# Performance work log

Measured on AMD Instinct MI355X. Metric: run time of the kernel, lower is better.

Reference implementation:

```python
import jax, jax.numpy as jnp
import numpy as np

L, P, DV, DP = 16, 1024, 64, 16   # latent caps, prim caps (neighbors), latent vec, prim vec
N_SRC, N_TGT = 64, 64
NUM_ITER = 3


def setup_inputs() -> dict:
    key = jax.random.key(0)
    k1, k2, k3 = jax.random.split(key, 3)
    feature = jax.random.normal(k1, (N_SRC + N_TGT, DP), dtype=jnp.float32)
    # neighbor indices: each half indexes into its own 64-row feature block
    select_cap = jax.random.randint(k2, (N_SRC + N_TGT, P), 0, N_SRC).astype(jnp.int64)
    W = 0.01 * jax.random.normal(k3, (L, P, DV, DP), dtype=jnp.float32)
    return {"feature": feature, "select_cap": select_cap, "W": W, "n_src": N_SRC}


def squash(s):
    # s: [..., DV]
    sn = jnp.sum(s * s, axis=-1, keepdims=True)
    return sn * s / ((1.0 + sn) * jnp.sqrt(sn))


def routing(x, W):
    # x: [B, P, DP], W: [L, P, DV, DP]
    u_hat = jnp.einsum('lpvq,bpq->blpv', W, x)          # [B, L, P, DV]
    u_det = jax.lax.stop_gradient(u_hat)                 # matches torch .detach()
    b = jnp.zeros(x.shape[:1] + (L, P), dtype=x.dtype)   # routing logits [B, L, P]
    for _ in range(NUM_ITER - 1):
        c = jax.nn.softmax(b, axis=1)                    # softmax over latent caps dim
        v = squash(jnp.einsum('blp,blpv->blv', c, u_det))
        b = b + jnp.einsum('blv,blpv->blp', v, u_det)
    c = jax.nn.softmax(b, axis=1)
    return squash(jnp.einsum('blp,blpv->blv', c, u_hat))  # [B, L, DV]


def reference(feature, select_cap, W, n_src):
    # per-point neighbor gather, honoring src/tgt split at n_src
    feat_src = feature[:n_src]
    feat_tgt = feature[n_src:]
    batch_src = feat_src[select_cap[:n_src]]             # [n_src, P, DP]
    batch_tgt = feat_tgt[select_cap[n_src:]]             # [n_tgt, P, DP]
    batch_feat = jnp.concatenate([batch_src, batch_tgt], axis=0)  # [N, P, DP]
    caps = routing(batch_feat, W)                        # [N, L, DV]
    norms = jnp.linalg.norm(caps, axis=-1).T             # [L, N]
    return caps, norms
```

## Files before the change

### kernel.cpp

```cpp
#include <hip/hip_runtime.h>
#include <hip/hip_fp16.h>

namespace {

constexpr int L_  = 16;
constexpr int P_  = 1024;
constexpr int DV_ = 64;
constexpr int DP_ = 16;
constexpr int B_  = 128;

constexpr size_t PB   = (size_t)P_ * B_;
constexpr size_t SLV  = (size_t)B_ * L_ * DV_;
constexpr size_t LPBT = (size_t)L_ * PB;

constexpr int KCH = 64;
constexpr int PPC = P_ / KCH;

typedef _Float16 f16;
typedef __attribute__((ext_vector_type(4)))  _Float16 f16x4;
typedef __attribute__((ext_vector_type(8)))  _Float16 f16x8;
typedef __attribute__((ext_vector_type(16))) float    f32x16;

constexpr size_t WF_UNITS = (size_t)L_ * P_ * 2 * 64;

__device__ __forceinline__ f16x8 mul_pk(const __half2 cwh, const f16x8 f) {
  union { f16x8 v; __half2 h2[4]; } fu, bu;
  fu.v = f;
#pragma unroll
  for (int i = 0; i < 4; ++i) bu.h2[i] = __hmul2(cwh, fu.h2[i]);
  return bu.v;
}

__global__ __launch_bounds__(256) void k_prepcvt(
    const float* __restrict__ W, const float* __restrict__ feat,
    const int* __restrict__ sel, const int* __restrict__ nsrc_p,
    f16* __restrict__ wf, f16* __restrict__ xq, f16* __restrict__ xqs)
{
  const int bid = blockIdx.x, tid = threadIdx.x;
  if (bid < 8192) {
    const int l   = bid & 15;
    const int rem = (bid >> 4) * 256 + tid;
    const int lane = rem & 63;
    const int mt   = (rem >> 6) & 1;
    const int p    = rem >> 7;
    const int v  = mt * 32 + (lane & 31);
    const int q8 = (lane >> 5) * 8;
    const float* src = W + (((size_t)l * P_ + p) * 64 + v) * 16 + q8;
    const float4 a = *(const float4*)src;
    const float4 b = *(const float4*)(src + 4);
    union { f16x8 v8; __half2 h2[4]; } o;
    o.h2[0] = __float22half2_rn(float2{a.x, a.y});
    o.h2[1] = __float22half2_rn(float2{a.z, a.w});
    o.h2[2] = __float22half2_rn(float2{b.x, b.y});
    o.h2[3] = __float22half2_rn(float2{b.z, b.w});
    reinterpret_cast<f16x8*>(wf)[(size_t)l * 131072 + rem] = o.v8;
  } else {
    const int id2 = (bid - 8192) * 256 + tid;
    const int p = id2 >> 7, b = id2 & 127;
    const int ns = *nsrc_p;
    const int j = sel[b * P_ + p] + (b >= ns ? ns : 0);
    const float4 f0 = *(const float4*)(feat + j * DP_);
    const float4 f1 = *(const float4*)(feat + j * DP_ + 4);
    const float4 f2 = *(const float4*)(feat + j * DP_ + 8);
    const float4 f3 = *(const float4*)(feat + j * DP_ + 12);
    union { f16x8 v8; __half2 h2[4]; } u0, u1, s0, s1;
    u0.h2[0] = __float22half2_rn(float2{f0.x, f0.y});
    u0.h2[1] = __float22half2_rn(float2{f0.z, f0.w});
    u0.h2[2] = __float22half2_rn(float2{f1.x, f1.y});
    u0.h2[3] = __float22half2_rn(float2{f1.z, f1.w});
    u1.h2[0] = __float22half2_rn(float2{f2.x, f2.y});
    u1.h2[1] = __float22half2_rn(float2{f2.z, f2.w});
    u1.h2[2] = __float22half2_rn(float2{f3.x, f3.y});
    u1.h2[3] = __float22half2_rn(float2{f3.z, f3.w});
    const __half2 sc = __float2half2_rn(0.0625f);
#pragma unroll
    for (int i = 0; i < 4; ++i) {
      s0.h2[i] = __hmul2(sc, u0.h2[i]);
      s1.h2[i] = __hmul2(sc, u1.h2[i]);
    }
    f16x8* xqu  = reinterpret_cast<f16x8*>(xq);
    f16x8* xqsu = reinterpret_cast<f16x8*>(xqs);
    xqu[(size_t)id2 * 2]      = u0.v8;
    xqu[(size_t)id2 * 2 + 1]  = u1.v8;
    xqsu[(size_t)id2 * 2]     = s0.v8;
    xqsu[(size_t)id2 * 2 + 1] = s1.v8;
  }
}

template<bool UNIFORM>
__global__ __launch_bounds__(256, 4) void k_wsum(
    const f16* __restrict__ wf, const f16* __restrict__ xq,
    const f16* __restrict__ xqs, const f16* __restrict__ cbuf,
    f16* __restrict__ spart)
{
  const int bid  = blockIdx.x;
  const int l    = bid & 15;
  const int kc   = bid >> 4;
  const int wave = threadIdx.x >> 6;
  const int lane = threadIdx.x & 63;
  const int col  = lane & 31;
  const int h    = lane >> 5;
  const int bcol = wave * 32 + col;

  f32x16 accA0, accA1, accB0, accB1;
#pragma unroll
  for (int r = 0; r < 16; ++r) {
    accA0[r] = 0.f; accA1[r] = 0.f; accB0[r] = 0.f; accB1[r] = 0.f;
  }

  const int p0 = kc * PPC;
  const f16x8* wfu = reinterpret_cast<const f16x8*>(wf);
  const f16x8* xqu = reinterpret_cast<const f16x8*>(UNIFORM ? xqs : xq);
#pragma unroll 4
  for (int ps = 0; ps < PPC; ++ps) {
    const int p = p0 + ps;
    const size_t lp = (size_t)l * P_ + p;

    f16x8 bfrag = xqu[(size_t)(p * B_ + bcol) * 2 + h];
    if (!UNIFORM) {
      const f16 cw = cbuf[(size_t)l * PB + (size_t)p * B_ + bcol];
      const __half hc = *reinterpret_cast<const __half*>(&cw);
      bfrag = mul_pk(__half2half2(hc), bfrag);
    }

    const f16x8 a0 = wfu[(lp * 2 + 0) * 64 + lane];
    const f16x8 a1 = wfu[(lp * 2 + 1) * 64 + lane];
    if (ps & 1) {
      accB0 = __builtin_amdgcn_mfma_f32_32x32x16_f16(a0, bfrag, accB0, 0, 0, 0);
      accB1 = __builtin_amdgcn_mfma_f32_32x32x16_f16(a1, bfrag, accB1, 0, 0, 0);
    } else {
      accA0 = __builtin_amdgcn_mfma_f32_32x32x16_f16(a0, bfrag, accA0, 0, 0, 0);
      accA1 = __builtin_amdgcn_mfma_f32_32x32x16_f16(a1, bfrag, accA1, 0, 0, 0);
    }
  }

  f16* op = spart + ((size_t)l * KCH + kc) * 8192 + (size_t)bcol * 64;
#pragma unroll
  for (int g = 0; g < 4; ++g) {
    f16x4 lo, hi;
#pragma unroll
    for (int j = 0; j < 4; ++j) {
      lo[j] = (f16)(accA0[g * 4 + j] + accB0[g * 4 + j]);
      hi[j] = (f16)(accA1[g * 4 + j] + accB1[g * 4 + j]);
    }
    *reinterpret_cast<f16x4*>(op + 8 * g + 4 * h)      = lo;
    *reinterpret_cast<f16x4*>(op + 32 + 8 * g + 4 * h) = hi;
  }
}

__global__ __launch_bounds__(256) void k_rsum(
    const f16* __restrict__ spart, float* __restrict__ sres)
{
  const int bid = blockIdx.x;
  const int l = bid & 15;
  const int r = bid >> 4;
  const int e = r * 1024 + threadIdx.x * 4;
  const f16* sp = spart + (size_t)l * KCH * 8192 + e;
  float a0 = 0.f, a1 = 0.f, a2 = 0.f, a3 = 0.f;
#pragma unroll
  for (int c = 0; c < KCH; ++c) {
    const f16x4 t = *reinterpret_cast<const f16x4*>(sp + (size_t)c * 8192);
    a0 += (float)t[0]; a1 += (float)t[1]; a2 += (float)t[2]; a3 += (float)t[3];
  }
  *reinterpret_cast<float4*>(sres + (size_t)l * 8192 + e) = float4{a0, a1, a2, a3};
}

template<bool ADDB>
__global__ __launch_bounds__(256, 4) void k_dotv(
    const f16* __restrict__ wf, const f16* __restrict__ xq,
    const float* __restrict__ sres, float* __restrict__ bb)
{
  const int bid  = blockIdx.x;
  const int l    = bid & 15;
  const int kc   = bid >> 4;
  const int wave = threadIdx.x >> 6;
  const int lane = threadIdx.x & 63;
  const int col  = lane & 31;
  const int h    = lane >> 5;
  const int bcol = wave * 32 + col;

  float vr0[16], vr1[16];
  float sn = 0.f;
  const float* vp = sres + (size_t)l * 8192 + (size_t)bcol * 64;
#pragma unroll
  for (int g = 0; g < 4; ++g) {
    const float4 lo = *reinterpret_cast<const float4*>(vp + 8 * g + 4 * h);
    const float4 hi = *reinterpret_cast<const float4*>(vp + 32 + 8 * g + 4 * h);
    vr0[g * 4 + 0] = lo.x; vr0[g * 4 + 1] = lo.y;
    vr0[g * 4 + 2] = lo.z; vr0[g * 4 + 3] = lo.w;
    vr1[g * 4 + 0] = hi.x; vr1[g * 4 + 1] = hi.y;
    vr1[g * 4 + 2] = hi.z; vr1[g * 4 + 3] = hi.w;
    sn += lo.x * lo.x + lo.y * lo.y + lo.z * lo.z + lo.w * lo.w;
    sn += hi.x * hi.x + hi.y * hi.y + hi.z * hi.z + hi.w * hi.w;
  }
  sn += __shfl_xor(sn, 32);
  const float scale = sqrtf(sn) / (1.f + sn);
#pragma unroll
  for (int r = 0; r < 16; ++r) { vr0[r] *= scale; vr1[r] *= scale; }

  f32x16 zz;
#pragma unroll
  for (int r = 0; r < 16; ++r) zz[r] = 0.f;

  const int p0 = kc * PPC;
  const f16x8* wfu = reinterpret_cast<const f16x8*>(wf);
  const f16x8* xqu = reinterpret_cast<const f16x8*>(xq);

#pragma unroll 2
  for (int ps = 0; ps < PPC; ++ps) {
    const int p = p0 + ps;
    const size_t lp = (size_t)l * P_ + p;

    const f16x8 bfrag = xqu[(size_t)(p * B_ + bcol) * 2 + h];
    const f16x8 a0 = wfu[(lp * 2 + 0) * 64 + lane];
    const f16x8 a1 = wfu[(lp * 2 + 1) * 64 + lane];
    const f32x16 u0 = __builtin_amdgcn_mfma_f32_32x32x16_f16(a0, bfrag, zz, 0, 0, 0);
    const f32x16 u1 = __builtin_amdgcn_mfma_f32_32x32x16_f16(a1, bfrag, zz, 0, 0, 0);

    float d = 0.f;
#pragma unroll
    for (int r = 0; r < 16; ++r) {
      d = fmaf(u0[r], vr0[r], d);
      d = fmaf(u1[r], vr1[r], d);
    }
    d += __shfl_xor(d, 32);
    if (h == 0) {
      const size_t o = (size_t)l * PB + (size_t)p * B_ + bcol;
      bb[o] = ADDB ? d + bb[o] : d;
    }
  }
}

__global__ __launch_bounds__(256) void k_softmax(
    const float* __restrict__ lin, f16* __restrict__ cout)
{
  const int idx = blockIdx.x * 256 + threadIdx.x;
  const float* ip = lin + idx;
  float x[L_];
  float m = -1e30f;
#pragma unroll
  for (int l = 0; l < L_; ++l) { x[l] = ip[(size_t)l * PB]; m = fmaxf(m, x[l]); }
  float den = 0.f;
#pragma unroll
  for (int l = 0; l < L_; ++l) { x[l] = __expf(x[l] - m); den += x[l]; }
  const float r = 1.f / den;
  f16* op = cout + idx;
#pragma unroll
  for (int l = 0; l < L_; ++l) op[(size_t)l * PB] = (f16)(x[l] * r);
}

__global__ __launch_bounds__(256) void k_squashF(
    const float* __restrict__ sres, float* __restrict__ caps,
    float* __restrict__ norms)
{
  const int bid = blockIdx.x;
  const int l = bid & 15;
  const int b = (bid >> 4) * 4 + (threadIdx.x >> 6);
  const int v = threadIdx.x & 63;

  const float x = sres[(size_t)l * 8192 + (size_t)b * 64 + v];
  float t2 = x * x;
#pragma unroll
  for (int m = 32; m >= 1; m >>= 1) t2 += __shfl_xor(t2, m, 64);
  const float scale = sqrtf(t2) / (1.f + t2);

  caps[((size_t)b * L_ + l) * DV_ + v] = x * scale;
  if (v == 0) norms[(size_t)l * B_ + b] = t2 / (1.f + t2);
}

}

extern "C" void kernel_launch(void* const* d_in, const int* in_sizes, int n_in,
                              void* d_out, int out_size, void* d_ws, size_t ws_size,
                              hipStream_t stream)
{
  (void)in_sizes; (void)n_in; (void)out_size; (void)ws_size;
  const float* feat   = (const float*)d_in[0];
  const int*   sel    = (const int*)d_in[1];
  const float* W      = (const float*)d_in[2];
  const int*   nsrc_p = (const int*)d_in[3];

  float* caps  = (float*)d_out;
  float* norms = caps + SLV;

  char* base = (char*)d_ws;
  f16*   wf     = (f16*)base;                         base += WF_UNITS * 8 * 2;
  f16*   spart  = (f16*)base;                         base += (size_t)L_ * KCH * 8192 * 2;
  float* sres   = (float*)base;                       base += (size_t)L_ * 8192 * 4;
  float* bb1    = (float*)base;                       base += LPBT * 4;
  f16*   cbuf16 = (f16*)base;                         base += LPBT * 2;
  f16*   xq     = (f16*)base;                         base += PB * DP_ * 2;
  f16*   xqs    = (f16*)base;

  const dim3 blk(256);
  const dim3 gP(8704);
  const dim3 gH(KCH * L_);
  const dim3 gRS(128);
  const dim3 gS(512);
  const dim3 gQ(512);

  k_prepcvt<<<gP, blk, 0, stream>>>(W, feat, sel, nsrc_p, wf, xq, xqs);

  k_wsum<true ><<<gH, blk, 0, stream>>>(wf, xq, xqs, nullptr, spart);
  k_rsum       <<<gRS, blk, 0, stream>>>(spart, sres);
  k_dotv<false><<<gH, blk, 0, stream>>>(wf, xq, sres, bb1);

  k_softmax    <<<gS, blk, 0, stream>>>(bb1, cbuf16);
  k_wsum<false><<<gH, blk, 0, stream>>>(wf, xq, xqs, cbuf16, spart);
  k_rsum       <<<gRS, blk, 0, stream>>>(spart, sres);
  k_dotv<true ><<<gH, blk, 0, stream>>>(wf, xq, sres, bb1);

  k_softmax    <<<gS, blk, 0, stream>>>(bb1, cbuf16);
  k_wsum<false><<<gH, blk, 0, stream>>>(wf, xq, xqs, cbuf16, spart);
  k_rsum       <<<gRS, blk, 0, stream>>>(spart, sres);
  k_squashF    <<<gQ, blk, 0, stream>>>(sres, caps, norms);
}
```

Measured before the change: 225.1 us.

## Drop pre-scaled feature copy, store routing logits in fp16, fuse final reduce with squash

The separate 1/16-scaled feature buffer is removed. The uniform first iteration now uses the unscaled features, and the 1/16 factor is applied to the summed vector when the first dot product runs. Routing logits are stored in fp16 rather than fp32, which halves the logit traffic in the dot and softmax kernels. The final partial-sum reduction is fused with the squash and norm output, removing one launch and the round trip through sres. It also reorders the prep kernel so the gather blocks come first. The risks are precision loss in the fp16 logits and possible overflow in the unscaled fp16 partial sums.

Result: faster. 220.4 us (-2.1%).

```diff
diff --git a/kernel.cpp b/kernel.cpp
--- a/kernel.cpp
+++ b/kernel.cpp
@@ -34,12 +34,34 @@
 __global__ __launch_bounds__(256) void k_prepcvt(
     const float* __restrict__ W, const float* __restrict__ feat,
     const int* __restrict__ sel, const int* __restrict__ nsrc_p,
-    f16* __restrict__ wf, f16* __restrict__ xq, f16* __restrict__ xqs)
+    f16* __restrict__ wf, f16* __restrict__ xq)
 {
   const int bid = blockIdx.x, tid = threadIdx.x;
-  if (bid < 8192) {
-    const int l   = bid & 15;
-    const int rem = (bid >> 4) * 256 + tid;
+  if (bid < 512) {
+    const int id2 = bid * 256 + tid;
+    const int p = id2 >> 7, b = id2 & 127;
+    const int ns = *nsrc_p;
+    const int j = sel[b * P_ + p] + (b >= ns ? ns : 0);
+    const float4 f0 = *(const float4*)(feat + j * DP_);
+    const float4 f1 = *(const float4*)(feat + j * DP_ + 4);
+    const float4 f2 = *(const float4*)(feat + j * DP_ + 8);
+    const float4 f3 = *(const float4*)(feat + j * DP_ + 12);
+    union { f16x8 v8; __half2 h2[4]; } u0, u1;
+    u0.h2[0] = __float22half2_rn(float2{f0.x, f0.y});
+    u0.h2[1] = __float22half2_rn(float2{f0.z, f0.w});
+    u0.h2[2] = __float22half2_rn(float2{f1.x, f1.y});
+    u0.h2[3] = __float22half2_rn(float2{f1.z, f1.w});
+    u1.h2[0] = __float22half2_rn(float2{f2.x, f2.y});
+    u1.h2[1] = __float22half2_rn(float2{f2.z, f2.w});
+    u1.h2[2] = __float22half2_rn(float2{f3.x, f3.y});
+    u1.h2[3] = __float22half2_rn(float2{f3.z, f3.w});
+    f16x8* xqu = reinterpret_cast<f16x8*>(xq);
+    xqu[(size_t)id2 * 2]     = u0.v8;
+    xqu[(size_t)id2 * 2 + 1] = u1.v8;
+  } else {
+    const int wid = bid - 512;
+    const int l   = wid & 15;
+    const int rem = (wid >> 4) * 256 + tid;
     const int lane = rem & 63;
     const int mt   = (rem >> 6) & 1;
     const int p    = rem >> 7;
@@ -54,44 +76,13 @@
     o.h2[2] = __float22half2_rn(float2{b.x, b.y});
     o.h2[3] = __float22half2_rn(float2{b.z, b.w});
     reinterpret_cast<f16x8*>(wf)[(size_t)l * 131072 + rem] = o.v8;
-  } else {
-    const int id2 = (bid - 8192) * 256 + tid;
-    const int p = id2 >> 7, b = id2 & 127;
-    const int ns = *nsrc_p;
-    const int j = sel[b * P_ + p] + (b >= ns ? ns : 0);
-    const float4 f0 = *(const float4*)(feat + j * DP_);
-    const float4 f1 = *(const float4*)(feat + j * DP_ + 4);
-    const float4 f2 = *(const float4*)(feat + j * DP_ + 8);
-    const float4 f3 = *(const float4*)(feat + j * DP_ + 12);
-    union { f16x8 v8; __half2 h2[4]; } u0, u1, s0, s1;
-    u0.h2[0] = __float22half2_rn(float2{f0.x, f0.y});
-    u0.h2[1] = __float22half2_rn(float2{f0.z, f0.w});
-    u0.h2[2] = __float22half2_rn(float2{f1.x, f1.y});
-    u0.h2[3] = __float22half2_rn(float2{f1.z, f1.w});
-    u1.h2[0] = __float22half2_rn(float2{f2.x, f2.y});
-    u1.h2[1] = __float22half2_rn(float2{f2.z, f2.w});
-    u1.h2[2] = __float22half2_rn(float2{f3.x, f3.y});
-    u1.h2[3] = __float22half2_rn(float2{f3.z, f3.w});
-    const __half2 sc = __float2half2_rn(0.0625f);
-#pragma unroll
-    for (int i = 0; i < 4; ++i) {
-      s0.h2[i] = __hmul2(sc, u0.h2[i]);
-      s1.h2[i] = __hmul2(sc, u1.h2[i]);
-    }
-    f16x8* xqu  = reinterpret_cast<f16x8*>(xq);
-    f16x8* xqsu = reinterpret_cast<f16x8*>(xqs);
-    xqu[(size_t)id2 * 2]      = u0.v8;
-    xqu[(size_t)id2 * 2 + 1]  = u1.v8;
-    xqsu[(size_t)id2 * 2]     = s0.v8;
-    xqsu[(size_t)id2 * 2 + 1] = s1.v8;
   }
 }
 
 template<bool UNIFORM>
 __global__ __launch_bounds__(256, 4) void k_wsum(
     const f16* __restrict__ wf, const f16* __restrict__ xq,
-    const f16* __restrict__ xqs, const f16* __restrict__ cbuf,
-    f16* __restrict__ spart)
+    const f16* __restrict__ cbuf, f16* __restrict__ spart)
 {
   const int bid  = blockIdx.x;
   const int l    = bid & 15;
@@ -110,7 +101,7 @@
 
   const int p0 = kc * PPC;
   const f16x8* wfu = reinterpret_cast<const f16x8*>(wf);
-  const f16x8* xqu = reinterpret_cast<const f16x8*>(UNIFORM ? xqs : xq);
+  const f16x8* xqu = reinterpret_cast<const f16x8*>(xq);
 #pragma unroll 4
   for (int ps = 0; ps < PPC; ++ps) {
     const int p = p0 + ps;
@@ -165,10 +156,10 @@
   *reinterpret_cast<float4*>(sres + (size_t)l * 8192 + e) = float4{a0, a1, a2, a3};
 }
 
-template<bool ADDB>
+template<bool ADDB, bool SCALE>
 __global__ __launch_bounds__(256, 4) void k_dotv(
     const f16* __restrict__ wf, const f16* __restrict__ xq,
-    const float* __restrict__ sres, float* __restrict__ bb)
+    const float* __restrict__ sres, f16* __restrict__ bb)
 {
   const int bid  = blockIdx.x;
   const int l    = bid & 15;
@@ -184,8 +175,12 @@
   const float* vp = sres + (size_t)l * 8192 + (size_t)bcol * 64;
 #pragma unroll
   for (int g = 0; g < 4; ++g) {
-    const float4 lo = *reinterpret_cast<const float4*>(vp + 8 * g + 4 * h);
-    const float4 hi = *reinterpret_cast<const float4*>(vp + 32 + 8 * g + 4 * h);
+    float4 lo = *reinterpret_cast<const float4*>(vp + 8 * g + 4 * h);
+    float4 hi = *reinterpret_cast<const float4*>(vp + 32 + 8 * g + 4 * h);
+    if (SCALE) {
+      lo.x *= 0.0625f; lo.y *= 0.0625f; lo.z *= 0.0625f; lo.w *= 0.0625f;
+      hi.x *= 0.0625f; hi.y *= 0.0625f; hi.z *= 0.0625f; hi.w *= 0.0625f;
+    }
     vr0[g * 4 + 0] = lo.x; vr0[g * 4 + 1] = lo.y;
     vr0[g * 4 + 2] = lo.z; vr0[g * 4 + 3] = lo.w;
     vr1[g * 4 + 0] = hi.x; vr1[g * 4 + 1] = hi.y;
@@ -226,20 +221,20 @@
     d += __shfl_xor(d, 32);
     if (h == 0) {
       const size_t o = (size_t)l * PB + (size_t)p * B_ + bcol;
-      bb[o] = ADDB ? d + bb[o] : d;
+      bb[o] = ADDB ? (f16)(d + (float)bb[o]) : (f16)d;
     }
   }
 }
 
 __global__ __launch_bounds__(256) void k_softmax(
-    const float* __restrict__ lin, f16* __restrict__ cout)
+    const f16* __restrict__ lin, f16* __restrict__ cout)
 {
   const int idx = blockIdx.x * 256 + threadIdx.x;
-  const float* ip = lin + idx;
+  const f16* ip = lin + idx;
   float x[L_];
   float m = -1e30f;
 #pragma unroll
-  for (int l = 0; l < L_; ++l) { x[l] = ip[(size_t)l * PB]; m = fmaxf(m, x[l]); }
+  for (int l = 0; l < L_; ++l) { x[l] = (float)ip[(size_t)l * PB]; m = fmaxf(m, x[l]); }
   float den = 0.f;
 #pragma unroll
   for (int l = 0; l < L_; ++l) { x[l] = __expf(x[l] - m); den += x[l]; }
@@ -249,23 +244,35 @@
   for (int l = 0; l < L_; ++l) op[(size_t)l * PB] = (f16)(x[l] * r);
 }
 
-__global__ __launch_bounds__(256) void k_squashF(
-    const float* __restrict__ sres, float* __restrict__ caps,
+__global__ __launch_bounds__(256) void k_rsumF(
+    const f16* __restrict__ spart, float* __restrict__ caps,
     float* __restrict__ norms)
 {
   const int bid = blockIdx.x;
   const int l = bid & 15;
-  const int b = (bid >> 4) * 4 + (threadIdx.x >> 6);
-  const int v = threadIdx.x & 63;
-
-  const float x = sres[(size_t)l * 8192 + (size_t)b * 64 + v];
-  float t2 = x * x;
-#pragma unroll
-  for (int m = 32; m >= 1; m >>= 1) t2 += __shfl_xor(t2, m, 64);
-  const float scale = sqrtf(t2) / (1.f + t2);
-
-  caps[((size_t)b * L_ + l) * DV_ + v] = x * scale;
-  if (v == 0) norms[(size_t)l * B_ + b] = t2 / (1.f + t2);
+  const int r = bid >> 4;
+  const int t = threadIdx.x;
+  const int e = r * 1024 + t * 4;
+  const int b = e >> 6;
+  const int v4 = e & 63;
+
+  const f16* sp = spart + (size_t)l * KCH * 8192 + e;
+  float a0 = 0.f, a1 = 0.f, a2 = 0.f, a3 = 0.f;
+#pragma unroll
+  for (int c = 0; c < KCH; ++c) {
+    const f16x4 q = *reinterpret_cast<const f16x4*>(sp + (size_t)c * 8192);
+    a0 += (float)q[0]; a1 += (float)q[1]; a2 += (float)q[2]; a3 += (float)q[3];
+  }
+
+  float sn = a0 * a0 + a1 * a1 + a2 * a2 + a3 * a3;
+#pragma unroll
+  for (int m = 1; m <= 8; m <<= 1) sn += __shfl_xor(sn, m, 64);
+  const float scale = sqrtf(sn) / (1.f + sn);
+
+  float* cp = caps + ((size_t)b * L_ + l) * DV_ + v4;
+  *reinterpret_cast<float4*>(cp) =
+      float4{a0 * scale, a1 * scale, a2 * scale, a3 * scale};
+  if ((t & 15) == 0) norms[(size_t)l * B_ + b] = sn / (1.f + sn);
 }
 
 }
@@ -284,34 +291,31 @@
   float* norms = caps + SLV;
 
   char* base = (char*)d_ws;
-  f16*   wf     = (f16*)base;                         base += WF_UNITS * 8 * 2;
-  f16*   spart  = (f16*)base;                         base += (size_t)L_ * KCH * 8192 * 2;
-  float* sres   = (float*)base;                       base += (size_t)L_ * 8192 * 4;
-  float* bb1    = (float*)base;                       base += LPBT * 4;
-  f16*   cbuf16 = (f16*)base;                         base += LPBT * 2;
-  f16*   xq     = (f16*)base;                         base += PB * DP_ * 2;
-  f16*   xqs    = (f16*)base;
+  f16*   wf     = (f16*)base;   base += WF_UNITS * 8 * 2;
+  f16*   spart  = (f16*)base;   base += (size_t)L_ * KCH * 8192 * 2;
+  float* sres   = (float*)base; base += (size_t)L_ * 8192 * 4;
+  f16*   bb1    = (f16*)base;   base += LPBT * 2;
+  f16*   cbuf16 = (f16*)base;   base += LPBT * 2;
+  f16*   xq     = (f16*)base;
 
   const dim3 blk(256);
   const dim3 gP(8704);
   const dim3 gH(KCH * L_);
   const dim3 gRS(128);
   const dim3 gS(512);
-  const dim3 gQ(512);
-
-  k_prepcvt<<<gP, blk, 0, stream>>>(W, feat, sel, nsrc_p, wf, xq, xqs);
-
-  k_wsum<true ><<<gH, blk, 0, stream>>>(wf, xq, xqs, nullptr, spart);
+
+  k_prepcvt<<<gP, blk, 0, stream>>>(W, feat, sel, nsrc_p, wf, xq);
+
+  k_wsum<true ><<<gH, blk, 0, stream>>>(wf, xq, nullptr, spart);
   k_rsum       <<<gRS, blk, 0, stream>>>(spart, sres);
-  k_dotv<false><<<gH, blk, 0, stream>>>(wf, xq, sres, bb1);
+  k_dotv<false, true><<<gH, blk, 0, stream>>>(wf, xq, sres, bb1);
 
   k_softmax    <<<gS, blk, 0, stream>>>(bb1, cbuf16);
-  k_wsum<false><<<gH, blk, 0, stream>>>(wf, xq, xqs, cbuf16, spart);
+  k_wsum<false><<<gH, blk, 0, stream>>>(wf, xq, cbuf16, spart);
   k_rsum       <<<gRS, blk, 0, stream>>>(spart, sres);
-  k_dotv<true ><<<gH, blk, 0, stream>>>(wf, xq, sres, bb1);
+  k_dotv<true, false><<<gH, blk, 0, stream>>>(wf, xq, sres, bb1);
 
   k_softmax    <<<gS, blk, 0, stream>>>(bb1, cbuf16);
-  k_wsum<false><<<gH, blk, 0, stream>>>(wf, xq, xqs, cbuf16, spart);
-  k_rsum       <<<gRS, blk, 0, stream>>>(spart, sres);
-  k_squashF    <<<gQ, blk, 0, stream>>>(sres, caps, norms);
-}
+  k_wsum<false><<<gH, blk, 0, stream>>>(wf, xq, cbuf16, spart);
+  k_rsumF      <<<gRS, blk, 0, stream>>>(spart, caps, norms);
+}
```
